# Optimization experiments

Hardware: AMD Instinct MI355X
Metric: run time of the kernel (lower is better)

Reference implementation:

```python
import jax, jax.numpy as jnp
import numpy as np

B = 4096
F_ST, F_DY, M = 20, 10, 50
E = 16
N_ST, N_DY = 100000, 1000000
F_ALL = F_ST + F_DY                      # 30 fields total
P = F_ALL * (F_ALL - 1) // 2             # 435 strict upper-triangular pairs
D_IN = P * E                             # 6960 MLP input dim
H = 512
BN_EPS = 1e-5


def _bn(x, g, b):
    # BatchNorm1d in training mode: biased batch variance (matches torch)
    m = jnp.mean(x, axis=0)
    v = jnp.var(x, axis=0)
    return g * (x - m) * jax.lax.rsqrt(v + BN_EPS) + b


def setup_inputs() -> dict:
    key = jax.random.key(0)
    ks = jax.random.split(key, 16)
    s_emb = 0.02
    inp = {
        "static_ids": jax.random.randint(ks[0], (B, F_ST), 0, N_ST),
        "dynamic_ids": jax.random.randint(ks[1], (B, F_DY, M), 0, N_DY),
        "dynamic_lengths": jax.random.randint(ks[2], (B, F_DY), 1, M + 1),
        "st_emb": jax.random.normal(ks[3], (N_ST, E), jnp.float32) * s_emb,
        "dy_emb": jax.random.normal(ks[4], (N_DY, E), jnp.float32) * s_emb,
        "st_lr": jax.random.normal(ks[5], (N_ST, 1), jnp.float32) * s_emb,
        "dy_lr": jax.random.normal(ks[6], (N_DY, 1), jnp.float32) * s_emb,
        "bias": jax.random.normal(ks[7], (1,), jnp.float32),
        "bn1_g": jnp.ones((D_IN,), jnp.float32), "bn1_b": jnp.zeros((D_IN,), jnp.float32),
        "W1": jax.random.normal(ks[8], (D_IN, H), jnp.float32) / np.sqrt(D_IN),
        "b1": jnp.zeros((H,), jnp.float32),
        "bn2_g": jnp.ones((H,), jnp.float32), "bn2_b": jnp.zeros((H,), jnp.float32),
        "W2": jax.random.normal(ks[9], (H, H), jnp.float32) / np.sqrt(H),
        "b2": jnp.zeros((H,), jnp.float32),
        "bn3_g": jnp.ones((H,), jnp.float32), "bn3_b": jnp.zeros((H,), jnp.float32),
        "W3": jax.random.normal(ks[10], (H, H), jnp.float32) / np.sqrt(H),
        "b3": jnp.zeros((H,), jnp.float32),
        "bn_out_g": jnp.ones((H,), jnp.float32), "bn_out_b": jnp.zeros((H,), jnp.float32),
        "W_out": jax.random.normal(ks[11], (H, 1), jnp.float32) / np.sqrt(H),
        "b_out": jnp.zeros((1,), jnp.float32),
    }
    return inp


def reference(static_ids, dynamic_ids, dynamic_lengths,
              st_emb, dy_emb, st_lr, dy_lr, bias,
              bn1_g, bn1_b, W1, b1,
              bn2_g, bn2_b, W2, b2,
              bn3_g, bn3_b, W3, b3,
              bn_out_g, bn_out_b, W_out, b_out):
    lengths = jnp.maximum(dynamic_lengths, 1)                       # guard avg div
    valid = (jnp.arange(M)[None, None, :] < lengths[:, :, None])    # [B,Fdy,M]
    valid_f = valid.astype(jnp.float32)

    # DyEmb (method='avg'): masked mean over list positions -> [B,Fdy,E]
    dyn_tab = dy_emb[dynamic_ids]                                   # [B,Fdy,M,E]
    dyn_embeddings = jnp.einsum('bfme,bfm->bfe', dyn_tab, valid_f) / lengths[..., None].astype(jnp.float32)
    # StEmb: plain lookup -> [B,Fst,E]
    st_embeddings = st_emb[static_ids]

    all_emb = jnp.concatenate([st_embeddings, dyn_embeddings], axis=1)  # [B,F_ALL,E]

    # Strict upper triangle pairs (static indices == the boolean mask in torch code)
    iu, ju = np.triu_indices(F_ALL, k=1)                            # each [P]
    combine = all_emb[:, iu, :] * all_emb[:, ju, :]                 # [B,P,E]
    x = combine.reshape(combine.shape[0], -1)                       # [B, P*E]

    # Linear parts: StEmb/DyEmb with embedding_size=1 (dyLr uses method='sum')
    static_lr_out = st_lr[static_ids][..., 0]                       # [B,Fst]
    dyn_lr_out = jnp.einsum('bfm,bfm->bf', dy_lr[dynamic_ids][..., 0], valid_f)  # [B,Fdy]

    # BN -> Linear -> ReLU tower
    h1 = _bn(x, bn1_g, bn1_b) @ W1 + b1
    h2 = _bn(jax.nn.relu(h1), bn2_g, bn2_b) @ W2 + b2
    out3 = _bn(jax.nn.relu(h2), bn3_g, bn3_b) @ W3 + b3             # embedding_lr_out_3
    # final BN+Linear is computed in torch but unused in scores (kept faithful)
    _ = _bn(jax.nn.relu(out3), bn_out_g, bn_out_b) @ W_out + b_out

    scores = (bias
              + jnp.sum(static_lr_out, axis=-1)
              + jnp.sum(dyn_lr_out, axis=-1)
              + jnp.sum(out3, axis=-1))                             # [B]
    return scores
```

## Files before the change

### kernel.cpp

```cpp
#include <hip/hip_runtime.h>

typedef __attribute__((ext_vector_type(8))) short short8;
typedef __attribute__((ext_vector_type(4))) float f32x4;

__device__ __forceinline__ unsigned short f2b(float f) {
    union { float f; unsigned u; } uf; uf.f = f;
    unsigned r = uf.u + 0x7fffu + ((uf.u >> 16) & 1u);
    return (unsigned short)(r >> 16);
}
__device__ __forceinline__ float b2f(unsigned short b) {
    union { unsigned u; float f; } uf; uf.u = ((unsigned)b) << 16;
    return uf.f;
}
__device__ __forceinline__ void gload_lds16(const void* g, void* l) {
    __builtin_amdgcn_global_load_lds(
        (const __attribute__((address_space(1))) void*)g,
        (__attribute__((address_space(3))) void*)l,
        16, 0, 0);
}

#define B_SZ 4096
#define F_ST 20
#define F_DY 10
#define MLEN 50
#define E_SZ 16
#define F_ALL 30
#define NPAIR 435
#define DIN 6960
#define KP 7168
#define H_SZ 512
#define BN_EPS 1e-5f

__global__ __launch_bounds__(256) void k_stemb(
    const int* __restrict__ st_ids, const float* __restrict__ st_emb,
    float* __restrict__ all_emb)
{
    int idx = blockIdx.x * 256 + threadIdx.x;
    int e4 = idx & 3, bf = idx >> 2;
    int b = bf / F_ST, f = bf % F_ST;
    int id = st_ids[bf];
    f32x4 v = *(const f32x4*)(st_emb + (long)id * E_SZ + e4 * 4);
    *(f32x4*)(all_emb + ((long)b * F_ALL + f) * E_SZ + e4 * 4) = v;
}

__global__ __launch_bounds__(512) void k_dyemb(
    const int* __restrict__ dy_ids, const int* __restrict__ dy_len,
    const float* __restrict__ dy_emb, float* __restrict__ all_emb)
{
    int gw = blockIdx.x * 8 + (threadIdx.x >> 6);
    int l = threadIdx.x & 63;
    int b = gw / F_DY, f = gw - b * F_DY;
    int len = dy_len[b * F_DY + f]; if (len < 1) len = 1;
    const int* ids = dy_ids + ((long)b * F_DY + f) * MLEN;
    int idv = (l < MLEN) ? ids[l] : 0;
    int e = l & 15, mq = l >> 4;
    float acc = 0.f;
#pragma unroll
    for (int j = 0; j < 13; ++j) {
        int m = mq + (j << 2);
        int id = __shfl(idv, m, 64);
        float v = (m < len) ? dy_emb[(long)id * E_SZ + e] : 0.f;
        acc += v;
    }
    acc += __shfl_xor(acc, 16, 64);
    acc += __shfl_xor(acc, 32, 64);
    if (l < 16)
        all_emb[((long)b * F_ALL + F_ST + f) * E_SZ + e] = acc / (float)len;
}

__global__ __launch_bounds__(512) void k_lr(
    const int* __restrict__ st_ids, const int* __restrict__ dy_ids,
    const int* __restrict__ dy_len, const float* __restrict__ st_lr,
    const float* __restrict__ dy_lr, const float* __restrict__ bias,
    float* __restrict__ lr_score)
{
    int w = threadIdx.x >> 6, l = threadIdx.x & 63;
    int b = blockIdx.x * 8 + w;
    float acc = 0.f;
    if (l < F_ST) acc += st_lr[st_ids[b * F_ST + l]];
#pragma unroll
    for (int i = 0; i < 8; ++i) {
        int idx = i * 64 + l;
        if (idx < F_DY * MLEN) {
            int f = idx / MLEN, m = idx - f * MLEN;
            int len = dy_len[b * F_DY + f]; if (len < 1) len = 1;
            if (m < len)
                acc += dy_lr[dy_ids[((long)b * F_DY + f) * MLEN + m]];
        }
    }
    for (int s = 32; s; s >>= 1) acc += __shfl_down(acc, s, 64);
    if (l == 0) lr_score[b] = bias[0] + acc;
}

__global__ __launch_bounds__(256) void k_x(
    const float* __restrict__ all_emb, unsigned short* __restrict__ x16,
    float* __restrict__ s1, float* __restrict__ s1q)
{
    __shared__ float es[16 * 480];
    __shared__ int pip[NPAIR], pjp[NPAIR];
    int t = threadIdx.x, b0 = blockIdx.x * 16;
    for (int p = t; p < NPAIR; p += 256) {
        int i = 0, rem = p;
        while (rem >= (F_ALL - 1) - i) { rem -= (F_ALL - 1) - i; ++i; }
        pip[p] = i; pjp[p] = i + 1 + rem;
    }
    for (int idx = t; idx < 16 * 480; idx += 256)
        es[idx] = all_emb[(long)b0 * 480 + idx];
    __syncthreads();

    int ci[28], cj[28];
#pragma unroll
    for (int k = 0; k < 28; ++k) {
        int d = t + (k << 8);
        if (d < DIN) {
            int p = d >> 4, e = d & 15;
            ci[k] = pip[p] * E_SZ + e;
            cj[k] = pjp[p] * E_SZ + e;
        } else { ci[k] = -1; cj[k] = 0; }
    }
    float sum[28], sq[28];
#pragma unroll
    for (int k = 0; k < 28; ++k) { sum[k] = 0.f; sq[k] = 0.f; }

    for (int r = 0; r < 16; ++r) {
        const float* row = &es[r * 480];
        long ob = (long)(b0 + r) * KP;
#pragma unroll
        for (int k = 0; k < 28; ++k) {
            int d = t + (k << 8);
            if (ci[k] >= 0) {
                float v = row[ci[k]] * row[cj[k]];
                unsigned short h = f2b(v);
                x16[ob + d] = h;
                float vb = b2f(h);
                sum[k] += vb; sq[k] += vb * vb;
            } else {
                x16[ob + d] = 0;
            }
        }
    }
#pragma unroll
    for (int k = 0; k < 28; ++k) {
        int d = t + (k << 8);
        if (ci[k] >= 0) { atomicAdd(&s1[d], sum[k]); atomicAdd(&s1q[d], sq[k]); }
    }
}

__global__ __launch_bounds__(256) void k_prep(
    const float* __restrict__ s, const float* __restrict__ sqs,
    const float* __restrict__ g, const float* __restrict__ bb,
    float* __restrict__ a, float* __restrict__ c,
    const float* __restrict__ W3, float* __restrict__ w3s)
{
    int t = threadIdx.x;
    if (blockIdx.x < 28) {
        int d = blockIdx.x * 256 + t;
        if (d < DIN) {
            float m = s[d] * (1.f / 4096.f);
            float var = sqs[d] * (1.f / 4096.f) - m * m;
            float av = g[d] * rsqrtf(var + BN_EPS);
            a[d] = av; c[d] = bb[d] - m * av;
        }
    } else {
        int row = (blockIdx.x - 28) * 16 + (t >> 4), sub = t & 15;
        float acc = 0.f;
        for (int i = 0; i < 32; ++i) acc += W3[(long)row * H_SZ + sub + i * 16];
#pragma unroll
        for (int sh = 8; sh; sh >>= 1) acc += __shfl_xor(acc, sh, 16);
        if (sub == 0) w3s[row] = acc;
    }
}

__global__ __launch_bounds__(256) void k_w1t(
    const float* __restrict__ W1, const float* __restrict__ a1,
    const float* __restrict__ c1, unsigned short* __restrict__ w1t,
    float* __restrict__ con)
{
    int gi = blockIdx.x * 256 + threadIdx.x;
    int kg = gi >> 9, n = gi & 511;
    short8 out; float cacc = 0.f;
#pragma unroll
    for (int i = 0; i < 8; ++i) {
        int k = kg * 8 + i;
        if (k < DIN) {
            float w = W1[(long)k * H_SZ + n];
            out[i] = (short)f2b(a1[k] * w);
            cacc += c1[k] * w;
        } else out[i] = 0;
    }
    *(short8*)(w1t + (long)n * KP + kg * 8) = out;
    atomicAdd(&con[n], cacc);
}

__global__ __launch_bounds__(512, 2) void k_gemm1(
    const unsigned short* __restrict__ A, const unsigned short* __restrict__ Bt,
    float* __restrict__ accbuf)
{
    __shared__ __align__(16) short As[64 * 64];
    __shared__ __align__(16) short Bs[512 * 64];
    const int t = threadIdx.x;
    const int w = t >> 6, l = t & 63;
    const int lm = l & 15, lq = l >> 4;
    const int row0 = blockIdx.x * 64;
    const int k0 = blockIdx.y * (KP / 8);

    const int srow = t >> 3;
    const int gch = (t & 7) ^ (srow & 7);
    const unsigned short* gA = A + (long)(row0 + srow) * KP + k0 + gch * 8;
    const unsigned short* gB = Bt + (long)srow * KP + k0 + gch * 8;
    short* AsW = As + w * 512;
    short* BsW = Bs + w * 512;

    f32x4 acc[4][4];
#pragma unroll
    for (int mi = 0; mi < 4; ++mi)
#pragma unroll
        for (int ni = 0; ni < 4; ++ni) acc[mi][ni] = (f32x4){0.f,0.f,0.f,0.f};

    for (int kt = 0; kt < 14; ++kt) {
        gload_lds16(gA, AsW);
#pragma unroll
        for (int c = 0; c < 8; ++c)
            gload_lds16(gB + (long)(64 * c) * KP, BsW + c * 4096);
        __syncthreads();
#pragma unroll
        for (int s = 0; s < 2; ++s) {
            short8 af[4];
#pragma unroll
            for (int mi = 0; mi < 4; ++mi) {
                int m = mi * 16 + lm;
                int sl = (s * 4 + lq) ^ (m & 7);
                af[mi] = *(const short8*)(As + m * 64 + sl * 8);
            }
#pragma unroll
            for (int ni = 0; ni < 4; ++ni) {
                int rb = w * 64 + ni * 16 + lm;
                int sl = (s * 4 + lq) ^ (rb & 7);
                short8 bf = *(const short8*)(Bs + rb * 64 + sl * 8);
#pragma unroll
                for (int mi = 0; mi < 4; ++mi)
                    acc[mi][ni] = __builtin_amdgcn_mfma_f32_16x16x32_bf16(
                        af[mi], bf, acc[mi][ni], 0, 0, 0);
            }
        }
        __syncthreads();
        gA += 64; gB += 64;
    }

#pragma unroll
    for (int ni = 0; ni < 4; ++ni) {
        int col = w * 64 + ni * 16 + lm;
#pragma unroll
        for (int mi = 0; mi < 4; ++mi) {
            int rbase = row0 + mi * 16 + lq * 4;
#pragma unroll
            for (int r = 0; r < 4; ++r)
                atomicAdd(&accbuf[(long)(rbase + r) * H_SZ + col], acc[mi][ni][r]);
        }
    }
}

__global__ __launch_bounds__(256) void k_ep(
    const float* __restrict__ accbuf, const float* __restrict__ con1,
    const float* __restrict__ b1, unsigned short* __restrict__ r1,
    float* __restrict__ s2, float* __restrict__ s2q)
{
    __shared__ float con[H_SZ];
    int t = threadIdx.x, r0 = blockIdx.x * 32;
    con[t] = b1[t] + con1[t];
    con[t + 256] = b1[t + 256] + con1[t + 256];
    __syncthreads();
    float a0 = 0.f, q0 = 0.f, a1v = 0.f, q1 = 0.f;
    for (int r = 0; r < 32; ++r) {
        long base = (long)(r0 + r) * H_SZ;
        float v0 = accbuf[base + t] + con[t];
        float v1 = accbuf[base + t + 256] + con[t + 256];
        v0 = v0 > 0.f ? v0 : 0.f;
        v1 = v1 > 0.f ? v1 : 0.f;
        unsigned short h0 = f2b(v0), h1 = f2b(v1);
        r1[base + t] = h0; r1[base + t + 256] = h1;
        float b0 = b2f(h0), b1f = b2f(h1);
        a0 += b0; q0 += b0 * b0; a1v += b1f; q1 += b1f * b1f;
    }
    atomicAdd(&s2[t], a0);        atomicAdd(&s2q[t], q0);
    atomicAdd(&s2[t + 256], a1v); atomicAdd(&s2q[t + 256], q1);
}

__global__ __launch_bounds__(256) void k_w2t(
    const float* __restrict__ W2, const float* __restrict__ s2,
    const float* __restrict__ s2q, const float* __restrict__ g2,
    const float* __restrict__ bb2, unsigned short* __restrict__ w2t,
    float* __restrict__ con)
{
    int gi = blockIdx.x * 256 + threadIdx.x;
    int kg = gi >> 9, n = gi & 511;
    short8 out; float cacc = 0.f;
#pragma unroll
    for (int i = 0; i < 8; ++i) {
        int k = kg * 8 + i;
        float m = s2[k] * (1.f / 4096.f);
        float var = s2q[k] * (1.f / 4096.f) - m * m;
        float av = g2[k] * rsqrtf(var + BN_EPS);
        float cv = bb2[k] - m * av;
        float w = W2[(long)k * H_SZ + n];
        out[i] = (short)f2b(av * w);
        cacc += cv * w;
    }
    *(short8*)(w2t + (long)n * H_SZ + kg * 8) = out;
    atomicAdd(&con[n], cacc);
}

__global__ __launch_bounds__(512) void k_gemm2(
    const unsigned short* __restrict__ A, const unsigned short* __restrict__ Bt,
    const float* __restrict__ cvec, const float* __restrict__ bvec,
    unsigned short* __restrict__ Out, float* __restrict__ ss,
    float* __restrict__ sq)
{
    const int Kp = H_SZ;
    __shared__ __align__(16) short As[128 * 32];
    __shared__ __align__(16) short Bs[64 * 32];
    const int t = threadIdx.x;
    const int w = t >> 6, l = t & 63;
    const int wm = w >> 1, wn = w & 1;
    const int lm = l & 15, lq = l >> 4;
    const int row0 = blockIdx.y * 128;
    const int col0 = blockIdx.x * 64;

    const unsigned short* gA = A + (long)(row0 + (t >> 2)) * Kp + ((t & 3) * 8);
    const unsigned short* gB = Bt + (long)(col0 + ((t >> 2) & 63)) * Kp + ((t & 3) * 8);
    short* AsW = As + w * 512;
    short* BsW = Bs + w * 512;

    const short* aBase0 = As + (wm * 32 + lm) * 32 + lq * 8;
    const short* aBase1 = aBase0 + 16 * 32;
    const short* bBase0 = Bs + (wn * 32 + lm) * 32 + lq * 8;
    const short* bBase1 = bBase0 + 16 * 32;

    f32x4 acc00 = {0.f,0.f,0.f,0.f}, acc01 = acc00, acc10 = acc00, acc11 = acc00;

    for (int kt = 0; kt < Kp / 32; ++kt) {
        gload_lds16(gA, AsW);
        if (t < 256) gload_lds16(gB, BsW);
        __syncthreads();
        short8 af0 = *(const short8*)aBase0;
        short8 af1 = *(const short8*)aBase1;
        short8 bf0 = *(const short8*)bBase0;
        short8 bf1 = *(const short8*)bBase1;
        acc00 = __builtin_amdgcn_mfma_f32_16x16x32_bf16(af0, bf0, acc00, 0, 0, 0);
        acc01 = __builtin_amdgcn_mfma_f32_16x16x32_bf16(af0, bf1, acc01, 0, 0, 0);
        acc10 = __builtin_amdgcn_mfma_f32_16x16x32_bf16(af1, bf0, acc10, 0, 0, 0);
        acc11 = __builtin_amdgcn_mfma_f32_16x16x32_bf16(af1, bf1, acc11, 0, 0, 0);
        __syncthreads();
        gA += 32; gB += 32;
    }

    f32x4 accs[2][2] = {{acc00, acc01}, {acc10, acc11}};
#pragma unroll
    for (int ni = 0; ni < 2; ++ni) {
        int col = col0 + wn * 32 + ni * 16 + lm;
        float cb = cvec[col] + bvec[col];
        float psum = 0.f, psq = 0.f;
#pragma unroll
        for (int mi = 0; mi < 2; ++mi) {
            int rbase = row0 + wm * 32 + mi * 16 + lq * 4;
#pragma unroll
            for (int r = 0; r < 4; ++r) {
                float v = accs[mi][ni][r] + cb;
                v = v > 0.f ? v : 0.f;
                unsigned short h = f2b(v);
                Out[(long)(rbase + r) * H_SZ + col] = h;
                float vb = b2f(h);
                psum += vb; psq += vb * vb;
            }
        }
        psum += __shfl_xor(psum, 16, 64); psum += __shfl_xor(psum, 32, 64);
        psq  += __shfl_xor(psq , 16, 64); psq  += __shfl_xor(psq , 32, 64);
        if (lq == 0) { atomicAdd(&ss[col], psum); atomicAdd(&sq[col], psq); }
    }
}

__global__ __launch_bounds__(256) void k_final(
    const unsigned short* __restrict__ r2, const float* __restrict__ s3,
    const float* __restrict__ s3q, const float* __restrict__ g3,
    const float* __restrict__ bb3, const float* __restrict__ w3s,
    const float* __restrict__ b3, const float* __restrict__ lr_score,
    float* __restrict__ out)
{
    int t = threadIdx.x, w = t >> 6, l = t & 63;
    int b = blockIdx.x * 4 + w;
    float acc = 0.f;
#pragma unroll
    for (int i = 0; i < 8; ++i) {
        int e = i * 64 + l;
        float m = s3[e] * (1.f / 4096.f);
        float var = s3q[e] * (1.f / 4096.f) - m * m;
        float a3 = g3[e] * rsqrtf(var + BN_EPS);
        float c3 = bb3[e] - m * a3;
        float v = a3 * b2f(r2[(long)b * H_SZ + e]) + c3;
        acc += v * w3s[e] + b3[e];
    }
    for (int s = 32; s; s >>= 1) acc += __shfl_down(acc, s, 64);
    if (l == 0) out[b] = lr_score[b] + acc;
}

extern "C" void kernel_launch(void* const* d_in, const int* in_sizes, int n_in,
                              void* d_out, int out_size, void* d_ws, size_t ws_size,
                              hipStream_t stream) {
    const int*   st_ids = (const int*)d_in[0];
    const int*   dy_ids = (const int*)d_in[1];
    const int*   dy_len = (const int*)d_in[2];
    const float* st_emb = (const float*)d_in[3];
    const float* dy_emb = (const float*)d_in[4];
    const float* st_lr  = (const float*)d_in[5];
    const float* dy_lr  = (const float*)d_in[6];
    const float* bias   = (const float*)d_in[7];
    const float* bn1_g  = (const float*)d_in[8];
    const float* bn1_b  = (const float*)d_in[9];
    const float* W1     = (const float*)d_in[10];
    const float* b1     = (const float*)d_in[11];
    const float* bn2_g  = (const float*)d_in[12];
    const float* bn2_b  = (const float*)d_in[13];
    const float* W2     = (const float*)d_in[14];
    const float* b2     = (const float*)d_in[15];
    const float* bn3_g  = (const float*)d_in[16];
    const float* bn3_b  = (const float*)d_in[17];
    const float* W3     = (const float*)d_in[18];
    const float* b3     = (const float*)d_in[19];

    char* ws = (char*)d_ws;
    size_t off = 0;
    auto alloc = [&](size_t bytes) -> char* {
        char* p = ws + off;
        off = (off + bytes + 255) & ~(size_t)255;
        return p;
    };
    char* R = alloc((size_t)B_SZ * H_SZ * 4);
    float*          all_emb = (float*)R;
    float*          accbuf  = (float*)R;
    unsigned short* r2      = (unsigned short*)R;

    unsigned short* x16     = (unsigned short*)alloc((size_t)B_SZ * KP * 2);
    unsigned short* w1t     = (unsigned short*)alloc((size_t)H_SZ * KP * 2);
    unsigned short* r1      = (unsigned short*)alloc((size_t)B_SZ * H_SZ * 2);
    unsigned short* w2t     = (unsigned short*)alloc((size_t)H_SZ * H_SZ * 2);
    float*          lr_sc   = (float*)alloc(B_SZ * 4);
    float* a1  = (float*)alloc(KP * 4);
    float* c1  = (float*)alloc(KP * 4);
    float* w3s = (float*)alloc(H_SZ * 4);
    char* zstart = ws + off;
    float* s1   = (float*)alloc(KP * 4);
    float* s1q  = (float*)alloc(KP * 4);
    float* con1 = (float*)alloc(H_SZ * 4);
    float* s2   = (float*)alloc(H_SZ * 4);
    float* s2q  = (float*)alloc(H_SZ * 4);
    float* con2 = (float*)alloc(H_SZ * 4);
    float* s3   = (float*)alloc(H_SZ * 4);
    float* s3q  = (float*)alloc(H_SZ * 4);
    size_t zbytes = (size_t)((ws + off) - zstart);

    hipMemsetAsync(zstart, 0, zbytes, stream);
    k_stemb<<<(B_SZ * F_ST * 4) / 256, 256, 0, stream>>>(st_ids, st_emb, all_emb);
    k_dyemb<<<(B_SZ * F_DY) / 8, 512, 0, stream>>>(dy_ids, dy_len, dy_emb, all_emb);
    k_lr<<<B_SZ / 8, 512, 0, stream>>>(st_ids, dy_ids, dy_len, st_lr, dy_lr,
                                       bias, lr_sc);
    k_x<<<B_SZ / 16, 256, 0, stream>>>(all_emb, x16, s1, s1q);
    hipMemsetAsync(R, 0, (size_t)B_SZ * H_SZ * 4, stream);
    k_prep<<<60, 256, 0, stream>>>(s1, s1q, bn1_g, bn1_b, a1, c1, W3, w3s);
    k_w1t<<<(896 * 512) / 256, 256, 0, stream>>>(W1, a1, c1, w1t, con1);
    k_gemm1<<<dim3(64, 8), 512, 0, stream>>>(x16, w1t, accbuf);
    k_ep<<<128, 256, 0, stream>>>(accbuf, con1, b1, r1, s2, s2q);
    k_w2t<<<128, 256, 0, stream>>>(W2, s2, s2q, bn2_g, bn2_b, w2t, con2);
    k_gemm2<<<dim3(8, 32), 512, 0, stream>>>(r1, w2t, con2, b2, r2, s3, s3q);
    k_final<<<B_SZ / 4, 256, 0, stream>>>(r2, s3, s3q, bn3_g, bn3_b, w3s, b3,
                                          lr_sc, (float*)d_out);
}
```

Before: 392.5 us.

## Merge gather kernels, retile GEMM1 to 128x128, replace W1 atomics with partials

The three embedding and linear-term gather kernels become one launch that dispatches on block index. GEMM1 moves from 64x512 tiles with K=64 steps and 512 threads to 128x128 tiles with K=32 steps, 256 threads and a higher occupancy bound, which gives a 4x32x8 grid with much less LDS per block. The W1 transpose kernel now writes per-K-block partial sums of the BN shift term instead of issuing atomics, and the epilogue reduces those 112 partials. This trades fewer launches and atomics, plus more parallel GEMM blocks, for more A-tile reloads and a small serial reduction in the epilogue.

```diff
diff --git a/kernel.cpp b/kernel.cpp
--- a/kernel.cpp
+++ b/kernel.cpp
@@ -28,68 +28,63 @@
 #define NPAIR 435
 #define DIN 6960
 #define KP 7168
+#define KB1 112
 #define H_SZ 512
 #define BN_EPS 1e-5f
 
-__global__ __launch_bounds__(256) void k_stemb(
-    const int* __restrict__ st_ids, const float* __restrict__ st_emb,
-    float* __restrict__ all_emb)
-{
-    int idx = blockIdx.x * 256 + threadIdx.x;
-    int e4 = idx & 3, bf = idx >> 2;
-    int b = bf / F_ST, f = bf % F_ST;
-    int id = st_ids[bf];
-    f32x4 v = *(const f32x4*)(st_emb + (long)id * E_SZ + e4 * 4);
-    *(f32x4*)(all_emb + ((long)b * F_ALL + f) * E_SZ + e4 * 4) = v;
-}
-
-__global__ __launch_bounds__(512) void k_dyemb(
-    const int* __restrict__ dy_ids, const int* __restrict__ dy_len,
-    const float* __restrict__ dy_emb, float* __restrict__ all_emb)
-{
-    int gw = blockIdx.x * 8 + (threadIdx.x >> 6);
-    int l = threadIdx.x & 63;
-    int b = gw / F_DY, f = gw - b * F_DY;
-    int len = dy_len[b * F_DY + f]; if (len < 1) len = 1;
-    const int* ids = dy_ids + ((long)b * F_DY + f) * MLEN;
-    int idv = (l < MLEN) ? ids[l] : 0;
-    int e = l & 15, mq = l >> 4;
-    float acc = 0.f;
-#pragma unroll
-    for (int j = 0; j < 13; ++j) {
-        int m = mq + (j << 2);
-        int id = __shfl(idv, m, 64);
-        float v = (m < len) ? dy_emb[(long)id * E_SZ + e] : 0.f;
-        acc += v;
-    }
-    acc += __shfl_xor(acc, 16, 64);
-    acc += __shfl_xor(acc, 32, 64);
-    if (l < 16)
-        all_emb[((long)b * F_ALL + F_ST + f) * E_SZ + e] = acc / (float)len;
-}
-
-__global__ __launch_bounds__(512) void k_lr(
+__global__ __launch_bounds__(512) void k_gather(
     const int* __restrict__ st_ids, const int* __restrict__ dy_ids,
-    const int* __restrict__ dy_len, const float* __restrict__ st_lr,
+    const int* __restrict__ dy_len, const float* __restrict__ st_emb,
+    const float* __restrict__ dy_emb, const float* __restrict__ st_lr,
     const float* __restrict__ dy_lr, const float* __restrict__ bias,
-    float* __restrict__ lr_score)
-{
-    int w = threadIdx.x >> 6, l = threadIdx.x & 63;
-    int b = blockIdx.x * 8 + w;
-    float acc = 0.f;
-    if (l < F_ST) acc += st_lr[st_ids[b * F_ST + l]];
-#pragma unroll
-    for (int i = 0; i < 8; ++i) {
-        int idx = i * 64 + l;
-        if (idx < F_DY * MLEN) {
-            int f = idx / MLEN, m = idx - f * MLEN;
-            int len = dy_len[b * F_DY + f]; if (len < 1) len = 1;
-            if (m < len)
-                acc += dy_lr[dy_ids[((long)b * F_DY + f) * MLEN + m]];
-        }
-    }
-    for (int s = 32; s; s >>= 1) acc += __shfl_down(acc, s, 64);
-    if (l == 0) lr_score[b] = bias[0] + acc;
+    float* __restrict__ all_emb, float* __restrict__ lr_score)
+{
+    int bid = blockIdx.x, t = threadIdx.x;
+    if (bid < 640) {
+        int idx = bid * 512 + t;
+        int e4 = idx & 3, bf = idx >> 2;
+        int b = bf / F_ST, f = bf % F_ST;
+        int id = st_ids[bf];
+        f32x4 v = *(const f32x4*)(st_emb + (long)id * E_SZ + e4 * 4);
+        *(f32x4*)(all_emb + ((long)b * F_ALL + f) * E_SZ + e4 * 4) = v;
+    } else if (bid < 5760) {
+        int gw = (bid - 640) * 8 + (t >> 6);
+        int l = t & 63;
+        int b = gw / F_DY, f = gw - b * F_DY;
+        int len = dy_len[b * F_DY + f]; if (len < 1) len = 1;
+        const int* ids = dy_ids + ((long)b * F_DY + f) * MLEN;
+        int idv = (l < MLEN) ? ids[l] : 0;
+        int e = l & 15, mq = l >> 4;
+        float acc = 0.f;
+#pragma unroll
+        for (int j = 0; j < 13; ++j) {
+            int m = mq + (j << 2);
+            int id = __shfl(idv, m, 64);
+            float v = (m < len) ? dy_emb[(long)id * E_SZ + e] : 0.f;
+            acc += v;
+        }
+        acc += __shfl_xor(acc, 16, 64);
+        acc += __shfl_xor(acc, 32, 64);
+        if (l < 16)
+            all_emb[((long)b * F_ALL + F_ST + f) * E_SZ + e] = acc / (float)len;
+    } else {
+        int w = t >> 6, l = t & 63;
+        int b = (bid - 5760) * 8 + w;
+        float acc = 0.f;
+        if (l < F_ST) acc += st_lr[st_ids[b * F_ST + l]];
+#pragma unroll
+        for (int i = 0; i < 8; ++i) {
+            int idx = i * 64 + l;
+            if (idx < F_DY * MLEN) {
+                int f = idx / MLEN, m = idx - f * MLEN;
+                int len = dy_len[b * F_DY + f]; if (len < 1) len = 1;
+                if (m < len)
+                    acc += dy_lr[dy_ids[((long)b * F_DY + f) * MLEN + m]];
+            }
+        }
+        for (int s = 32; s; s >>= 1) acc += __shfl_down(acc, s, 64);
+        if (l == 0) lr_score[b] = bias[0] + acc;
+    }
 }
 
 __global__ __launch_bounds__(256) void k_x(
@@ -174,42 +169,54 @@
 __global__ __launch_bounds__(256) void k_w1t(
     const float* __restrict__ W1, const float* __restrict__ a1,
     const float* __restrict__ c1, unsigned short* __restrict__ w1t,
-    float* __restrict__ con)
-{
-    int gi = blockIdx.x * 256 + threadIdx.x;
-    int kg = gi >> 9, n = gi & 511;
-    short8 out; float cacc = 0.f;
+    float* __restrict__ conp)
+{
+    int t = threadIdx.x;
+    int n = blockIdx.x * 256 + t;
+    int kb = blockIdx.y;
+    float cacc = 0.f;
 #pragma unroll
     for (int i = 0; i < 8; ++i) {
-        int k = kg * 8 + i;
-        if (k < DIN) {
-            float w = W1[(long)k * H_SZ + n];
-            out[i] = (short)f2b(a1[k] * w);
-            cacc += c1[k] * w;
-        } else out[i] = 0;
-    }
-    *(short8*)(w1t + (long)n * KP + kg * 8) = out;
-    atomicAdd(&con[n], cacc);
-}
-
-__global__ __launch_bounds__(512, 2) void k_gemm1(
+        int kg = kb * 8 + i;
+        short8 o;
+#pragma unroll
+        for (int j = 0; j < 8; ++j) {
+            int k = kg * 8 + j;
+            if (k < DIN) {
+                float w = W1[(long)k * H_SZ + n];
+                o[j] = (short)f2b(a1[k] * w);
+                cacc += c1[k] * w;
+            } else o[j] = 0;
+        }
+        *(short8*)(w1t + (long)n * KP + kg * 8) = o;
+    }
+    conp[kb * H_SZ + n] = cacc;
+}
+
+__global__ __launch_bounds__(256, 4) void k_gemm1(
     const unsigned short* __restrict__ A, const unsigned short* __restrict__ Bt,
     float* __restrict__ accbuf)
 {
-    __shared__ __align__(16) short As[64 * 64];
-    __shared__ __align__(16) short Bs[512 * 64];
+    __shared__ __align__(16) short As[128 * 32];
+    __shared__ __align__(16) short Bs[128 * 32];
     const int t = threadIdx.x;
     const int w = t >> 6, l = t & 63;
+    const int wm = w >> 1, wn = w & 1;
     const int lm = l & 15, lq = l >> 4;
-    const int row0 = blockIdx.x * 64;
-    const int k0 = blockIdx.y * (KP / 8);
-
-    const int srow = t >> 3;
-    const int gch = (t & 7) ^ (srow & 7);
-    const unsigned short* gA = A + (long)(row0 + srow) * KP + k0 + gch * 8;
-    const unsigned short* gB = Bt + (long)srow * KP + k0 + gch * 8;
-    short* AsW = As + w * 512;
-    short* BsW = Bs + w * 512;
+    const int col0 = blockIdx.x * 128;
+    const int row0 = blockIdx.y * 128;
+    const int k0 = blockIdx.z * (KP / 8);
+
+    const int srow = w * 16 + (l >> 2);
+    const int sc0 = ((l & 3) - (l >> 3)) & 3;
+    const unsigned short* gA0 = A + (long)(row0 + srow) * KP + k0 + sc0 * 8;
+    const unsigned short* gA1 = A + (long)(row0 + 64 + srow) * KP + k0 + sc0 * 8;
+    const unsigned short* gB0 = Bt + (long)(col0 + srow) * KP + k0 + sc0 * 8;
+    const unsigned short* gB1 = Bt + (long)(col0 + 64 + srow) * KP + k0 + sc0 * 8;
+    short* AsW0 = As + w * 512;
+    short* AsW1 = As + 2048 + w * 512;
+    short* BsW0 = Bs + w * 512;
+    short* BsW1 = Bs + 2048 + w * 512;
 
     f32x4 acc[4][4];
 #pragma unroll
@@ -217,42 +224,39 @@
 #pragma unroll
         for (int ni = 0; ni < 4; ++ni) acc[mi][ni] = (f32x4){0.f,0.f,0.f,0.f};
 
-    for (int kt = 0; kt < 14; ++kt) {
-        gload_lds16(gA, AsW);
-#pragma unroll
-        for (int c = 0; c < 8; ++c)
-            gload_lds16(gB + (long)(64 * c) * KP, BsW + c * 4096);
+    for (int kt = 0; kt < 28; ++kt) {
+        gload_lds16(gA0, AsW0);
+        gload_lds16(gA1, AsW1);
+        gload_lds16(gB0, BsW0);
+        gload_lds16(gB1, BsW1);
         __syncthreads();
-#pragma unroll
-        for (int s = 0; s < 2; ++s) {
-            short8 af[4];
-#pragma unroll
-            for (int mi = 0; mi < 4; ++mi) {
-                int m = mi * 16 + lm;
-                int sl = (s * 4 + lq) ^ (m & 7);
-                af[mi] = *(const short8*)(As + m * 64 + sl * 8);
-            }
-#pragma unroll
-            for (int ni = 0; ni < 4; ++ni) {
-                int rb = w * 64 + ni * 16 + lm;
-                int sl = (s * 4 + lq) ^ (rb & 7);
-                short8 bf = *(const short8*)(Bs + rb * 64 + sl * 8);
-#pragma unroll
-                for (int mi = 0; mi < 4; ++mi)
-                    acc[mi][ni] = __builtin_amdgcn_mfma_f32_16x16x32_bf16(
-                        af[mi], bf, acc[mi][ni], 0, 0, 0);
-            }
+        short8 af[4];
+#pragma unroll
+        for (int mi = 0; mi < 4; ++mi) {
+            int m = wm * 64 + mi * 16 + lm;
+            int sl = (lq + (m >> 1)) & 3;
+            af[mi] = *(const short8*)(As + m * 32 + sl * 8);
+        }
+#pragma unroll
+        for (int ni = 0; ni < 4; ++ni) {
+            int rb = wn * 64 + ni * 16 + lm;
+            int sl = (lq + (rb >> 1)) & 3;
+            short8 bf = *(const short8*)(Bs + rb * 32 + sl * 8);
+#pragma unroll
+            for (int mi = 0; mi < 4; ++mi)
+                acc[mi][ni] = __builtin_amdgcn_mfma_f32_16x16x32_bf16(
+                    af[mi], bf, acc[mi][ni], 0, 0, 0);
         }
         __syncthreads();
-        gA += 64; gB += 64;
+        gA0 += 32; gA1 += 32; gB0 += 32; gB1 += 32;
     }
 
 #pragma unroll
     for (int ni = 0; ni < 4; ++ni) {
-        int col = w * 64 + ni * 16 + lm;
+        int col = col0 + wn * 64 + ni * 16 + lm;
 #pragma unroll
         for (int mi = 0; mi < 4; ++mi) {
-            int rbase = row0 + mi * 16 + lq * 4;
+            int rbase = row0 + wm * 64 + mi * 16 + lq * 4;
 #pragma unroll
             for (int r = 0; r < 4; ++r)
                 atomicAdd(&accbuf[(long)(rbase + r) * H_SZ + col], acc[mi][ni][r]);
@@ -261,14 +265,18 @@
 }
 
 __global__ __launch_bounds__(256) void k_ep(
-    const float* __restrict__ accbuf, const float* __restrict__ con1,
+    const float* __restrict__ accbuf, const float* __restrict__ conp,
     const float* __restrict__ b1, unsigned short* __restrict__ r1,
     float* __restrict__ s2, float* __restrict__ s2q)
 {
     __shared__ float con[H_SZ];
     int t = threadIdx.x, r0 = blockIdx.x * 32;
-    con[t] = b1[t] + con1[t];
-    con[t + 256] = b1[t + 256] + con1[t + 256];
+    float c0 = b1[t], c1v = b1[t + 256];
+    for (int p = 0; p < KB1; ++p) {
+        c0  += conp[p * H_SZ + t];
+        c1v += conp[p * H_SZ + t + 256];
+    }
+    con[t] = c0; con[t + 256] = c1v;
     __syncthreads();
     float a0 = 0.f, q0 = 0.f, a1v = 0.f, q1 = 0.f;
     for (int r = 0; r < 32; ++r) {
@@ -444,13 +452,13 @@
     unsigned short* r1      = (unsigned short*)alloc((size_t)B_SZ * H_SZ * 2);
     unsigned short* w2t     = (unsigned short*)alloc((size_t)H_SZ * H_SZ * 2);
     float*          lr_sc   = (float*)alloc(B_SZ * 4);
+    float*          conp    = (float*)alloc((size_t)KB1 * H_SZ * 4);
     float* a1  = (float*)alloc(KP * 4);
     float* c1  = (float*)alloc(KP * 4);
     float* w3s = (float*)alloc(H_SZ * 4);
     char* zstart = ws + off;
     float* s1   = (float*)alloc(KP * 4);
     float* s1q  = (float*)alloc(KP * 4);
-    float* con1 = (float*)alloc(H_SZ * 4);
     float* s2   = (float*)alloc(H_SZ * 4);
     float* s2q  = (float*)alloc(H_SZ * 4);
     float* con2 = (float*)alloc(H_SZ * 4);
@@ -459,16 +467,14 @@
     size_t zbytes = (size_t)((ws + off) - zstart);
 
     hipMemsetAsync(zstart, 0, zbytes, stream);
-    k_stemb<<<(B_SZ * F_ST * 4) / 256, 256, 0, stream>>>(st_ids, st_emb, all_emb);
-    k_dyemb<<<(B_SZ * F_DY) / 8, 512, 0, stream>>>(dy_ids, dy_len, dy_emb, all_emb);
-    k_lr<<<B_SZ / 8, 512, 0, stream>>>(st_ids, dy_ids, dy_len, st_lr, dy_lr,
-                                       bias, lr_sc);
+    k_gather<<<6272, 512, 0, stream>>>(st_ids, dy_ids, dy_len, st_emb, dy_emb,
+                                       st_lr, dy_lr, bias, all_emb, lr_sc);
     k_x<<<B_SZ / 16, 256, 0, stream>>>(all_emb, x16, s1, s1q);
     hipMemsetAsync(R, 0, (size_t)B_SZ * H_SZ * 4, stream);
     k_prep<<<60, 256, 0, stream>>>(s1, s1q, bn1_g, bn1_b, a1, c1, W3, w3s);
-    k_w1t<<<(896 * 512) / 256, 256, 0, stream>>>(W1, a1, c1, w1t, con1);
-    k_gemm1<<<dim3(64, 8), 512, 0, stream>>>(x16, w1t, accbuf);
-    k_ep<<<128, 256, 0, stream>>>(accbuf, con1, b1, r1, s2, s2q);
+    k_w1t<<<dim3(2, KB1), 256, 0, stream>>>(W1, a1, c1, w1t, conp);
+    k_gemm1<<<dim3(4, 32, 8), 256, 0, stream>>>(x16, w1t, accbuf);
+    k_ep<<<128, 256, 0, stream>>>(accbuf, conp, b1, r1, s2, s2q);
     k_w2t<<<128, 256, 0, stream>>>(W2, s2, s2q, bn2_g, bn2_b, w2t, con2);
     k_gemm2<<<dim3(8, 32), 512, 0, stream>>>(r1, w2t, con2, b2, r2, s3, s3q);
     k_final<<<B_SZ / 4, 256, 0, stream>>>(r2, s3, s3q, bn3_g, bn3_b, w3s, b3,
```

New measurement: 396.2 us. About the same (+0.9%).
